# Performance work log

Measured on AMD Instinct MI355X. Metric: run time of the kernel, lower is better.

## Reference

```python
import jax, jax.numpy as jnp
import numpy as np

NUM_EXPERTS = 256
TOP_K = 8
N_GROUP = 8
TOPK_GROUP = 4
ROUTED_SCALING = 2.5
EXPERTS_PER_GROUP = NUM_EXPERTS // N_GROUP  # 32


def setup_inputs() -> dict:
    key = jax.random.key(0)
    k1, k2, k3 = jax.random.split(key, 3)
    hidden_states = jax.random.normal(k1, (8192, 7168), dtype=jnp.float32)
    weight = jax.random.normal(k2, (NUM_EXPERTS, 7168), dtype=jnp.float32) * 0.02
    e_score_correction_bias = jax.random.normal(k3, (NUM_EXPERTS,), dtype=jnp.float32) * 0.1
    return {
        "hidden_states": hidden_states,
        "weight": weight,
        "e_score_correction_bias": e_score_correction_bias,
    }


def reference(hidden_states, weight, e_score_correction_bias):
    # Router logits: [T, E]
    router_logits = jnp.einsum("th,eh->te", hidden_states, weight)
    scores = jax.nn.sigmoid(router_logits)
    scores_for_choice = scores + e_score_correction_bias  # [T, E]

    T = scores_for_choice.shape[0]
    # Group-limited selection (noaux_tc): group score = sum of top-2 experts in group
    grouped = scores_for_choice.reshape(T, N_GROUP, EXPERTS_PER_GROUP)
    group_top2, _ = jax.lax.top_k(grouped, 2)            # [T, G, 2]
    group_scores = group_top2.sum(axis=-1)               # [T, G]
    _, group_idx = jax.lax.top_k(group_scores, TOPK_GROUP)  # [T, topk_group]
    group_mask = jax.nn.one_hot(group_idx, N_GROUP, dtype=scores.dtype).max(axis=1)  # [T, G]
    expert_mask = jnp.repeat(group_mask, EXPERTS_PER_GROUP, axis=-1)  # [T, E]
    masked_scores = scores_for_choice * expert_mask

    # Final top-k experts; routing weights gathered from raw sigmoid scores
    _, selected_experts = jax.lax.top_k(masked_scores, TOP_K)         # [T, K] int32
    routing_weights = jnp.take_along_axis(scores, selected_experts, axis=-1)  # [T, K]
    routing_weights = routing_weights / (routing_weights.sum(axis=-1, keepdims=True) + 1e-20)
    routing_weights = routing_weights * ROUTED_SCALING
    return routing_weights, selected_experts
```

## Files before the change

### kernel.cpp

```cpp
#include <hip/hip_runtime.h>
#include <math.h>
#include <stdint.h>

#define T_TOK 8192
#define NEXP  256
#define HD    7168
#define PLANE ((size_t)T_TOK * NEXP)
#define SCALE 4096.0f
#define INV_S2 (1.0f / 16777216.0f)
#define BM 128
#define BK 32
#define NSTEP_TOT (HD / BK)
#define BIMG_STEP 32768

typedef _Float16 h8  __attribute__((ext_vector_type(8)));
typedef float f32x16 __attribute__((ext_vector_type(16)));
typedef __attribute__((address_space(3))) uint8_t       lds_t;
typedef __attribute__((address_space(1))) const uint8_t gbl_t;

__global__ __launch_bounds__(256) void wconv(const float* __restrict__ W,
                                             _Float16* __restrict__ img) {
  const int cc  = blockIdx.x * 256 + threadIdx.x;
  const int t   = cc >> 11;
  const int c   = cc & 2047;
  const int hl  = c >> 10;
  const int rem = c & 1023;
  const int row = rem >> 2;
  const int sp  = rem & 3;
  const int sl  = sp ^ ((row >> 1) & 3);
  const int k   = t * BK + sl * 8;

  const float* src = W + (size_t)row * HD + k;
  const float4 v0 = *(const float4*)src;
  const float4 v1 = *(const float4*)(src + 4);
  const float xs[8] = {v0.x, v0.y, v0.z, v0.w, v1.x, v1.y, v1.z, v1.w};
  h8 out;
#pragma unroll
  for (int j = 0; j < 8; ++j) {
    const float v = xs[j] * SCALE;
    const _Float16 hh = (_Float16)v;
    out[j] = hl ? (_Float16)(v - (float)hh) : hh;
  }
  *(h8*)(img + (size_t)cc * 8) = out;
}

__global__ __launch_bounds__(512) void router_gemm(
    const float* __restrict__ X, const _Float16* __restrict__ img,
    float* __restrict__ partial, int S) {
  __shared__ __align__(1024) _Float16 As[2][2][BM][BK];
  __shared__ __align__(1024) _Float16 Bs[2][2][NEXP][BK];

  const int tid = threadIdx.x;
  const int id  = blockIdx.x;
  const int sb  = id % S;
  const int mb  = id / S;

  const int row0  = mb * BM;
  const int nstep = (HD / S) / BK;
  const int tbase = sb * nstep;

  const int lane = tid & 63, wv = tid >> 6;
  const int wm = wv >> 2, wn = wv & 3;
  const int r31 = lane & 31, kg = lane >> 5;

  const int sm = tid >> 2;
  const int sk = tid & 3;
  const int spA = sk ^ ((sm >> 1) & 3);

  const float* Ap = X + (size_t)(row0 + sm) * HD + tbase * BK + sk * 8;
  const uint8_t* imgB = (const uint8_t*)img + (size_t)tbase * BIMG_STEP + tid * 16;

  f32x16 acc[2][2];
#pragma unroll
  for (int i = 0; i < 2; ++i)
#pragma unroll
    for (int j = 0; j < 2; ++j) acc[i][j] = (f32x16)(0.f);

#define STAGE_B(t, b)                                                          \
  {                                                                            \
    const uint8_t* g = imgB + (size_t)(t) * BIMG_STEP;                         \
    uint8_t* l = (uint8_t*)&Bs[b][0][0][0] + tid * 16;                         \
    _Pragma("unroll")                                                          \
    for (int i = 0; i < 4; ++i)                                                \
      __builtin_amdgcn_global_load_lds((gbl_t*)(uintptr_t)(g + i * 8192),      \
                                       (lds_t*)(uintptr_t)(l + i * 8192),      \
                                       16, 0, 0);                              \
  }

  STAGE_B(0, 0);
  {
    const float4 a0 = *(const float4*)(Ap);
    const float4 a1 = *(const float4*)(Ap + 4);
    const float xs[8] = {a0.x, a0.y, a0.z, a0.w, a1.x, a1.y, a1.z, a1.w};
    h8 hv, lv;
#pragma unroll
    for (int j = 0; j < 8; ++j) {
      const float v = xs[j] * SCALE;
      const _Float16 hh = (_Float16)v;
      hv[j] = hh; lv[j] = (_Float16)(v - (float)hh);
    }
    *(h8*)&As[0][0][sm][spA * 8] = hv;
    *(h8*)&As[0][1][sm][spA * 8] = lv;
  }

  for (int t = 0; t < nstep; ++t) {
    const int cur = t & 1;
    __syncthreads();

    const bool more = (t + 1 < nstep);
    float4 a0, a1;
    if (more) {
      STAGE_B(t + 1, cur ^ 1);
      a0 = *(const float4*)(Ap + (size_t)(t + 1) * BK);
      a1 = *(const float4*)(Ap + (size_t)(t + 1) * BK + 4);
    }

#pragma unroll
    for (int ks = 0; ks < 2; ++ks) {
      h8 aH[2], aL[2], bH[2], bL[2];
#pragma unroll
      for (int mi = 0; mi < 2; ++mi) {
        const int row = wm * 64 + mi * 32 + r31;
        const int sp  = (ks * 2 + kg) ^ ((row >> 1) & 3);
        aH[mi] = *(const h8*)&As[cur][0][row][sp * 8];
        aL[mi] = *(const h8*)&As[cur][1][row][sp * 8];
      }
#pragma unroll
      for (int ni = 0; ni < 2; ++ni) {
        const int col = wn * 64 + ni * 32 + r31;
        const int sp  = (ks * 2 + kg) ^ ((col >> 1) & 3);
        bH[ni] = *(const h8*)&Bs[cur][0][col][sp * 8];
        bL[ni] = *(const h8*)&Bs[cur][1][col][sp * 8];
      }
#pragma unroll
      for (int mi = 0; mi < 2; ++mi)
#pragma unroll
        for (int ni = 0; ni < 2; ++ni) {
          acc[mi][ni] = __builtin_amdgcn_mfma_f32_32x32x16_f16(aH[mi], bH[ni], acc[mi][ni], 0, 0, 0);
          acc[mi][ni] = __builtin_amdgcn_mfma_f32_32x32x16_f16(aL[mi], bH[ni], acc[mi][ni], 0, 0, 0);
          acc[mi][ni] = __builtin_amdgcn_mfma_f32_32x32x16_f16(aH[mi], bL[ni], acc[mi][ni], 0, 0, 0);
        }
    }

    if (more) {
      const int nb = cur ^ 1;
      const float xs[8] = {a0.x, a0.y, a0.z, a0.w, a1.x, a1.y, a1.z, a1.w};
      h8 hv, lv;
#pragma unroll
      for (int j = 0; j < 8; ++j) {
        const float v = xs[j] * SCALE;
        const _Float16 hh = (_Float16)v;
        hv[j] = hh; lv[j] = (_Float16)(v - (float)hh);
      }
      *(h8*)&As[nb][0][sm][spA * 8] = hv;
      *(h8*)&As[nb][1][sm][spA * 8] = lv;
    }
  }

  float* base = partial + (size_t)sb * PLANE;
#pragma unroll
  for (int mi = 0; mi < 2; ++mi)
#pragma unroll
    for (int ni = 0; ni < 2; ++ni) {
      const int col = wn * 64 + ni * 32 + r31;
#pragma unroll
      for (int reg = 0; reg < 16; ++reg) {
        const int rr  = (reg & 3) + 8 * (reg >> 2) + 4 * kg;
        const int row = row0 + wm * 64 + mi * 32 + rr;
        base[(size_t)row * NEXP + col] = acc[mi][ni][reg];
      }
    }
}

__global__ __launch_bounds__(256) void gate_kernel(const float* __restrict__ logits,
                                                   const float* __restrict__ bias,
                                                   float* __restrict__ out_w,
                                                   float* __restrict__ out_e, int S) {
    const int wave = threadIdx.x >> 6;
    const int lane = threadIdx.x & 63;
    const int t = blockIdx.x * 4 + wave;
    if (t >= T_TOK) return;

    float l4[4] = {0.f, 0.f, 0.f, 0.f};
    for (int s = 0; s < S; ++s) {
        const float4 v = *(const float4*)(&logits[(size_t)s * PLANE + (size_t)t * NEXP + lane * 4]);
        l4[0] += v.x; l4[1] += v.y; l4[2] += v.z; l4[3] += v.w;
    }
    const float4 bv = *(const float4*)(&bias[lane * 4]);

    float s4[4], c[4];
#pragma unroll
    for (int j = 0; j < 4; ++j) s4[j] = 1.f / (1.f + expf(-l4[j] * INV_S2));
    c[0] = s4[0] + bv.x;
    c[1] = s4[1] + bv.y;
    c[2] = s4[2] + bv.z;
    c[3] = s4[3] + bv.w;

    float a = fmaxf(c[0], c[1]), b = fminf(c[0], c[1]);
    float d = fmaxf(c[2], c[3]), e = fminf(c[2], c[3]);
    float m1 = fmaxf(a, d);
    float m2 = fmaxf(fminf(a, d), fmaxf(b, e));
#pragma unroll
    for (int off = 1; off < 8; off <<= 1) {
        const float o1 = __shfl_xor(m1, off);
        const float o2 = __shfl_xor(m2, off);
        const float n1 = fmaxf(m1, o1);
        const float n2 = fmaxf(fminf(m1, o1), fmaxf(m2, o2));
        m1 = n1; m2 = n2;
    }
    const float gs = m1 + m2;
    const int   g  = lane >> 3;

    int rank = 0;
#pragma unroll
    for (int gg = 0; gg < 8; ++gg) {
        const float og = __shfl(gs, gg * 8);
        rank += (og > gs) || (og == gs && gg < g);
    }
    const bool gsel = rank < 4;

    float v[4];
#pragma unroll
    for (int j = 0; j < 4; ++j) v[j] = gsel ? c[j] : 0.0f;

    float selw = 0.f;
    int   seli = 0;
    float wsum = 0.f;

#pragma unroll
    for (int k = 0; k < 8; ++k) {
        float bvv = v[0]; int bi = lane * 4; float br = s4[0];
#pragma unroll
        for (int j = 1; j < 4; ++j) {
            if (v[j] > bvv) { bvv = v[j]; bi = lane * 4 + j; br = s4[j]; }
        }
#pragma unroll
        for (int off = 32; off > 0; off >>= 1) {
            const float ov = __shfl_xor(bvv, off);
            const int   oi = __shfl_xor(bi, off);
            const float orr = __shfl_xor(br, off);
            if (ov > bvv || (ov == bvv && oi < bi)) { bvv = ov; bi = oi; br = orr; }
        }
        if (lane == k) { selw = br; seli = bi; }
        wsum += br;
        const int rem = bi - lane * 4;
#pragma unroll
        for (int j = 0; j < 4; ++j)
            if (rem == j) v[j] = -INFINITY;
    }

    if (lane < 8) {
        const float w = selw / (wsum + 1e-20f) * 2.5f;
        out_w[(size_t)t * 8 + lane] = w;
        out_e[(size_t)t * 8 + lane] = (float)seli;
    }
}

extern "C" void kernel_launch(void* const* d_in, const int* in_sizes, int n_in,
                              void* d_out, int out_size, void* d_ws, size_t ws_size,
                              hipStream_t stream) {
    const float* X    = (const float*)d_in[0];
    const float* W    = (const float*)d_in[1];
    const float* bias = (const float*)d_in[2];
    float* out = (float*)d_out;

    _Float16* img = (_Float16*)d_ws;
    const size_t woff = (size_t)NSTEP_TOT * BIMG_STEP;
    float* partial = (float*)((char*)d_ws + woff);

    int S = 1;
    if (ws_size >= woff + 4 * PLANE * sizeof(float)) S = 4;
    else if (ws_size >= woff + 2 * PLANE * sizeof(float)) S = 2;

    wconv<<<dim3(NSTEP_TOT * 2048 / 256), 256, 0, stream>>>(W, img);
    router_gemm<<<dim3((T_TOK / BM) * S), 512, 0, stream>>>(X, img, partial, S);
    gate_kernel<<<dim3(T_TOK / 4), 256, 0, stream>>>(partial, bias, out, out + (size_t)T_TOK * 8, S);
}
```

Before: 129.5 us.

## Split router GEMM tile along N into two 128-wide blocks with split accumulators

```diff
diff --git a/kernel.cpp b/kernel.cpp
--- a/kernel.cpp
+++ b/kernel.cpp
@@ -9,6 +9,7 @@
 #define SCALE 4096.0f
 #define INV_S2 (1.0f / 16777216.0f)
 #define BM 128
+#define BN 128
 #define BK 32
 #define NSTEP_TOT (HD / BK)
 #define BIMG_STEP 32768
@@ -23,14 +24,14 @@
   const int cc  = blockIdx.x * 256 + threadIdx.x;
   const int t   = cc >> 11;
   const int c   = cc & 2047;
-  const int hl  = c >> 10;
-  const int rem = c & 1023;
-  const int row = rem >> 2;
-  const int sp  = rem & 3;
+  const int nb  = c >> 10;
+  const int hl  = (c >> 9) & 1;
+  const int row = (c >> 2) & 127;
+  const int sp  = c & 3;
   const int sl  = sp ^ ((row >> 1) & 3);
   const int k   = t * BK + sl * 8;
 
-  const float* src = W + (size_t)row * HD + k;
+  const float* src = W + (size_t)(nb * 128 + row) * HD + k;
   const float4 v0 = *(const float4*)src;
   const float4 v1 = *(const float4*)(src + 4);
   const float xs[8] = {v0.x, v0.y, v0.z, v0.w, v1.x, v1.y, v1.z, v1.w};
@@ -44,37 +45,37 @@
   *(h8*)(img + (size_t)cc * 8) = out;
 }
 
-__global__ __launch_bounds__(512) void router_gemm(
+__global__ __launch_bounds__(256, 2) void router_gemm(
     const float* __restrict__ X, const _Float16* __restrict__ img,
     float* __restrict__ partial, int S) {
   __shared__ __align__(1024) _Float16 As[2][2][BM][BK];
-  __shared__ __align__(1024) _Float16 Bs[2][2][NEXP][BK];
+  __shared__ __align__(1024) _Float16 Bs[2][2][BN][BK];
 
   const int tid = threadIdx.x;
   const int id  = blockIdx.x;
   const int sb  = id % S;
-  const int mb  = id / S;
+  const int nb  = (id / S) & 1;
+  const int mb  = id / (2 * S);
 
   const int row0  = mb * BM;
   const int nstep = (HD / S) / BK;
   const int tbase = sb * nstep;
 
   const int lane = tid & 63, wv = tid >> 6;
-  const int wm = wv >> 2, wn = wv & 3;
+  const int wm = wv >> 1, wn = wv & 1;
   const int r31 = lane & 31, kg = lane >> 5;
 
-  const int sm = tid >> 2;
-  const int sk = tid & 3;
-  const int spA = sk ^ ((sm >> 1) & 3);
-
-  const float* Ap = X + (size_t)(row0 + sm) * HD + tbase * BK + sk * 8;
-  const uint8_t* imgB = (const uint8_t*)img + (size_t)tbase * BIMG_STEP + tid * 16;
-
-  f32x16 acc[2][2];
+  const int sm = tid >> 1;
+  const int sk = tid & 1;
+
+  const float* Ap = X + (size_t)(row0 + sm) * HD + tbase * BK + sk * 16;
+  const uint8_t* imgB = (const uint8_t*)img + (size_t)tbase * BIMG_STEP + nb * 16384 + tid * 16;
+
+  f32x16 accP[2][2], accQ[2][2];
 #pragma unroll
   for (int i = 0; i < 2; ++i)
 #pragma unroll
-    for (int j = 0; j < 2; ++j) acc[i][j] = (f32x16)(0.f);
+    for (int j = 0; j < 2; ++j) { accP[i][j] = (f32x16)(0.f); accQ[i][j] = (f32x16)(0.f); }
 
 #define STAGE_B(t, b)                                                          \
   {                                                                            \
@@ -82,25 +83,34 @@
     uint8_t* l = (uint8_t*)&Bs[b][0][0][0] + tid * 16;                         \
     _Pragma("unroll")                                                          \
     for (int i = 0; i < 4; ++i)                                                \
-      __builtin_amdgcn_global_load_lds((gbl_t*)(uintptr_t)(g + i * 8192),      \
-                                       (lds_t*)(uintptr_t)(l + i * 8192),      \
+      __builtin_amdgcn_global_load_lds((gbl_t*)(uintptr_t)(g + i * 4096),      \
+                                       (lds_t*)(uintptr_t)(l + i * 4096),      \
                                        16, 0, 0);                              \
+  }
+
+#define CVT_WRITE(b, s, va, vb)                                                \
+  {                                                                            \
+    const float xs[8] = {va.x, va.y, va.z, va.w, vb.x, vb.y, vb.z, vb.w};      \
+    h8 hv, lv_;                                                                \
+    _Pragma("unroll")                                                          \
+    for (int j = 0; j < 8; ++j) {                                              \
+      const float v = xs[j] * SCALE;                                           \
+      const _Float16 hh = (_Float16)v;                                         \
+      hv[j] = hh; lv_[j] = (_Float16)(v - (float)hh);                          \
+    }                                                                          \
+    const int spp = (s) ^ ((sm >> 1) & 3);                                     \
+    *(h8*)&As[b][0][sm][spp * 8] = hv;                                         \
+    *(h8*)&As[b][1][sm][spp * 8] = lv_;                                        \
   }
 
   STAGE_B(0, 0);
   {
     const float4 a0 = *(const float4*)(Ap);
     const float4 a1 = *(const float4*)(Ap + 4);
-    const float xs[8] = {a0.x, a0.y, a0.z, a0.w, a1.x, a1.y, a1.z, a1.w};
-    h8 hv, lv;
-#pragma unroll
-    for (int j = 0; j < 8; ++j) {
-      const float v = xs[j] * SCALE;
-      const _Float16 hh = (_Float16)v;
-      hv[j] = hh; lv[j] = (_Float16)(v - (float)hh);
-    }
-    *(h8*)&As[0][0][sm][spA * 8] = hv;
-    *(h8*)&As[0][1][sm][spA * 8] = lv;
+    const float4 a2 = *(const float4*)(Ap + 8);
+    const float4 a3 = *(const float4*)(Ap + 12);
+    CVT_WRITE(0, sk * 2,     a0, a1);
+    CVT_WRITE(0, sk * 2 + 1, a2, a3);
   }
 
   for (int t = 0; t < nstep; ++t) {
@@ -108,11 +118,14 @@
     __syncthreads();
 
     const bool more = (t + 1 < nstep);
-    float4 a0, a1;
+    float4 a0, a1, a2, a3;
     if (more) {
+      const float* ap = Ap + (size_t)(t + 1) * BK;
+      a0 = *(const float4*)(ap);
+      a1 = *(const float4*)(ap + 4);
+      a2 = *(const float4*)(ap + 8);
+      a3 = *(const float4*)(ap + 12);
       STAGE_B(t + 1, cur ^ 1);
-      a0 = *(const float4*)(Ap + (size_t)(t + 1) * BK);
-      a1 = *(const float4*)(Ap + (size_t)(t + 1) * BK + 4);
     }
 
 #pragma unroll
@@ -132,28 +145,29 @@
         bH[ni] = *(const h8*)&Bs[cur][0][col][sp * 8];
         bL[ni] = *(const h8*)&Bs[cur][1][col][sp * 8];
       }
+      __builtin_amdgcn_s_setprio(1);
 #pragma unroll
       for (int mi = 0; mi < 2; ++mi)
 #pragma unroll
-        for (int ni = 0; ni < 2; ++ni) {
-          acc[mi][ni] = __builtin_amdgcn_mfma_f32_32x32x16_f16(aH[mi], bH[ni], acc[mi][ni], 0, 0, 0);
-          acc[mi][ni] = __builtin_amdgcn_mfma_f32_32x32x16_f16(aL[mi], bH[ni], acc[mi][ni], 0, 0, 0);
-          acc[mi][ni] = __builtin_amdgcn_mfma_f32_32x32x16_f16(aH[mi], bL[ni], acc[mi][ni], 0, 0, 0);
-        }
+        for (int ni = 0; ni < 2; ++ni)
+          accP[mi][ni] = __builtin_amdgcn_mfma_f32_32x32x16_f16(aH[mi], bH[ni], accP[mi][ni], 0, 0, 0);
+#pragma unroll
+      for (int mi = 0; mi < 2; ++mi)
+#pragma unroll
+        for (int ni = 0; ni < 2; ++ni)
+          accQ[mi][ni] = __builtin_amdgcn_mfma_f32_32x32x16_f16(aL[mi], bH[ni], accQ[mi][ni], 0, 0, 0);
+#pragma unroll
+      for (int mi = 0; mi < 2; ++mi)
+#pragma unroll
+        for (int ni = 0; ni < 2; ++ni)
+          accQ[mi][ni] = __builtin_amdgcn_mfma_f32_32x32x16_f16(aH[mi], bL[ni], accQ[mi][ni], 0, 0, 0);
+      __builtin_amdgcn_s_setprio(0);
     }
 
     if (more) {
-      const int nb = cur ^ 1;
-      const float xs[8] = {a0.x, a0.y, a0.z, a0.w, a1.x, a1.y, a1.z, a1.w};
-      h8 hv, lv;
-#pragma unroll
-      for (int j = 0; j < 8; ++j) {
-        const float v = xs[j] * SCALE;
-        const _Float16 hh = (_Float16)v;
-        hv[j] = hh; lv[j] = (_Float16)(v - (float)hh);
-      }
-      *(h8*)&As[nb][0][sm][spA * 8] = hv;
-      *(h8*)&As[nb][1][sm][spA * 8] = lv;
+      const int nbuf = cur ^ 1;
+      CVT_WRITE(nbuf, sk * 2,     a0, a1);
+      CVT_WRITE(nbuf, sk * 2 + 1, a2, a3);
     }
   }
 
@@ -162,12 +176,13 @@
   for (int mi = 0; mi < 2; ++mi)
 #pragma unroll
     for (int ni = 0; ni < 2; ++ni) {
-      const int col = wn * 64 + ni * 32 + r31;
+      const f32x16 acc = accP[mi][ni] + accQ[mi][ni];
+      const int col = nb * BN + wn * 64 + ni * 32 + r31;
 #pragma unroll
       for (int reg = 0; reg < 16; ++reg) {
         const int rr  = (reg & 3) + 8 * (reg >> 2) + 4 * kg;
         const int row = row0 + wm * 64 + mi * 32 + rr;
-        base[(size_t)row * NEXP + col] = acc[mi][ni][reg];
+        base[(size_t)row * NEXP + col] = acc[reg];
       }
     }
 }
@@ -273,6 +288,6 @@
     else if (ws_size >= woff + 2 * PLANE * sizeof(float)) S = 2;
 
     wconv<<<dim3(NSTEP_TOT * 2048 / 256), 256, 0, stream>>>(W, img);
-    router_gemm<<<dim3((T_TOK / BM) * S), 512, 0, stream>>>(X, img, partial, S);
+    router_gemm<<<dim3((T_TOK / BM) * 2 * S), 256, 0, stream>>>(X, img, partial, S);
     gate_kernel<<<dim3(T_TOK / 4), 256, 0, stream>>>(partial, bias, out, out + (size_t)T_TOK * 8, S);
 }
```

Measured after the change: 145.7 us. +12.5%, slower.

## Restructure router GEMM main loop with split accumulators and explicit wait scheduling

Applied to the files above, without the earlier changes.

```diff
diff --git a/kernel.cpp b/kernel.cpp
--- a/kernel.cpp
+++ b/kernel.cpp
@@ -44,7 +44,7 @@
   *(h8*)(img + (size_t)cc * 8) = out;
 }
 
-__global__ __launch_bounds__(512) void router_gemm(
+__global__ __launch_bounds__(512, 2) void router_gemm(
     const float* __restrict__ X, const _Float16* __restrict__ img,
     float* __restrict__ partial, int S) {
   __shared__ __align__(1024) _Float16 As[2][2][BM][BK];
@@ -70,11 +70,11 @@
   const float* Ap = X + (size_t)(row0 + sm) * HD + tbase * BK + sk * 8;
   const uint8_t* imgB = (const uint8_t*)img + (size_t)tbase * BIMG_STEP + tid * 16;
 
-  f32x16 acc[2][2];
+  f32x16 accP[2][2], accQ[2][2];
 #pragma unroll
   for (int i = 0; i < 2; ++i)
 #pragma unroll
-    for (int j = 0; j < 2; ++j) acc[i][j] = (f32x16)(0.f);
+    for (int j = 0; j < 2; ++j) { accP[i][j] = (f32x16)(0.f); accQ[i][j] = (f32x16)(0.f); }
 
 #define STAGE_B(t, b)                                                          \
   {                                                                            \
@@ -87,74 +87,100 @@
                                        16, 0, 0);                              \
   }
 
-  STAGE_B(0, 0);
+#define CVT_WRITE_A(b, va, vb)                                                 \
+  {                                                                            \
+    const float xs[8] = {va.x, va.y, va.z, va.w, vb.x, vb.y, vb.z, vb.w};      \
+    h8 hv, lv_;                                                                \
+    _Pragma("unroll")                                                          \
+    for (int j = 0; j < 8; ++j) {                                              \
+      const float v = xs[j] * SCALE;                                           \
+      const _Float16 hh = (_Float16)v;                                         \
+      hv[j] = hh; lv_[j] = (_Float16)(v - (float)hh);                          \
+    }                                                                          \
+    *(h8*)&As[b][0][sm][spA * 8] = hv;                                         \
+    *(h8*)&As[b][1][sm][spA * 8] = lv_;                                        \
+  }
+
   {
     const float4 a0 = *(const float4*)(Ap);
     const float4 a1 = *(const float4*)(Ap + 4);
-    const float xs[8] = {a0.x, a0.y, a0.z, a0.w, a1.x, a1.y, a1.z, a1.w};
-    h8 hv, lv;
-#pragma unroll
-    for (int j = 0; j < 8; ++j) {
-      const float v = xs[j] * SCALE;
-      const _Float16 hh = (_Float16)v;
-      hv[j] = hh; lv[j] = (_Float16)(v - (float)hh);
-    }
-    *(h8*)&As[0][0][sm][spA * 8] = hv;
-    *(h8*)&As[0][1][sm][spA * 8] = lv;
+    __builtin_amdgcn_sched_barrier(0);
+    STAGE_B(0, 0);
+    asm volatile("s_waitcnt vmcnt(0)" ::: "memory");
+    __builtin_amdgcn_sched_barrier(0);
+    CVT_WRITE_A(0, a0, a1);
+    asm volatile("s_waitcnt lgkmcnt(0)" ::: "memory");
+    __builtin_amdgcn_s_barrier();
   }
 
   for (int t = 0; t < nstep; ++t) {
     const int cur = t & 1;
-    __syncthreads();
-
+    const int nxt = cur ^ 1;
     const bool more = (t + 1 < nstep);
+
     float4 a0, a1;
     if (more) {
-      STAGE_B(t + 1, cur ^ 1);
-      a0 = *(const float4*)(Ap + (size_t)(t + 1) * BK);
-      a1 = *(const float4*)(Ap + (size_t)(t + 1) * BK + 4);
-    }
-
+      const float* ap = Ap + (size_t)(t + 1) * BK;
+      a0 = *(const float4*)(ap);
+      a1 = *(const float4*)(ap + 4);
+      __builtin_amdgcn_sched_barrier(0);
+      STAGE_B(t + 1, nxt);
+      __builtin_amdgcn_sched_barrier(0);
+      asm volatile("s_waitcnt vmcnt(6)" ::: "memory");
+    } else {
+      asm volatile("s_waitcnt vmcnt(0)" ::: "memory");
+    }
+    __builtin_amdgcn_sched_barrier(0);
+
+    h8 aH[2][2], aL[2][2], bH[2][2], bL[2][2];
 #pragma unroll
     for (int ks = 0; ks < 2; ++ks) {
-      h8 aH[2], aL[2], bH[2], bL[2];
 #pragma unroll
       for (int mi = 0; mi < 2; ++mi) {
         const int row = wm * 64 + mi * 32 + r31;
         const int sp  = (ks * 2 + kg) ^ ((row >> 1) & 3);
-        aH[mi] = *(const h8*)&As[cur][0][row][sp * 8];
-        aL[mi] = *(const h8*)&As[cur][1][row][sp * 8];
+        aH[ks][mi] = *(const h8*)&As[cur][0][row][sp * 8];
+        aL[ks][mi] = *(const h8*)&As[cur][1][row][sp * 8];
       }
 #pragma unroll
       for (int ni = 0; ni < 2; ++ni) {
         const int col = wn * 64 + ni * 32 + r31;
         const int sp  = (ks * 2 + kg) ^ ((col >> 1) & 3);
-        bH[ni] = *(const h8*)&Bs[cur][0][col][sp * 8];
-        bL[ni] = *(const h8*)&Bs[cur][1][col][sp * 8];
+        bH[ks][ni] = *(const h8*)&Bs[cur][0][col][sp * 8];
+        bL[ks][ni] = *(const h8*)&Bs[cur][1][col][sp * 8];
       }
+    }
+    asm volatile("s_waitcnt lgkmcnt(0)" ::: "memory");
+    __builtin_amdgcn_sched_barrier(0);
+
+    __builtin_amdgcn_s_setprio(1);
+#pragma unroll
+    for (int ks = 0; ks < 2; ++ks) {
 #pragma unroll
       for (int mi = 0; mi < 2; ++mi)
 #pragma unroll
-        for (int ni = 0; ni < 2; ++ni) {
-          acc[mi][ni] = __builtin_amdgcn_mfma_f32_32x32x16_f16(aH[mi], bH[ni], acc[mi][ni], 0, 0, 0);
-          acc[mi][ni] = __builtin_amdgcn_mfma_f32_32x32x16_f16(aL[mi], bH[ni], acc[mi][ni], 0, 0, 0);
-          acc[mi][ni] = __builtin_amdgcn_mfma_f32_32x32x16_f16(aH[mi], bL[ni], acc[mi][ni], 0, 0, 0);
-        }
-    }
+        for (int ni = 0; ni < 2; ++ni)
+          accP[mi][ni] = __builtin_amdgcn_mfma_f32_32x32x16_f16(aH[ks][mi], bH[ks][ni], accP[mi][ni], 0, 0, 0);
+#pragma unroll
+      for (int mi = 0; mi < 2; ++mi)
+#pragma unroll
+        for (int ni = 0; ni < 2; ++ni)
+          accQ[mi][ni] = __builtin_amdgcn_mfma_f32_32x32x16_f16(aL[ks][mi], bH[ks][ni], accQ[mi][ni], 0, 0, 0);
+#pragma unroll
+      for (int mi = 0; mi < 2; ++mi)
+#pragma unroll
+        for (int ni = 0; ni < 2; ++ni)
+          accQ[mi][ni] = __builtin_amdgcn_mfma_f32_32x32x16_f16(aH[ks][mi], bL[ks][ni], accQ[mi][ni], 0, 0, 0);
+    }
+    __builtin_amdgcn_s_setprio(0);
 
     if (more) {
-      const int nb = cur ^ 1;
-      const float xs[8] = {a0.x, a0.y, a0.z, a0.w, a1.x, a1.y, a1.z, a1.w};
-      h8 hv, lv;
-#pragma unroll
-      for (int j = 0; j < 8; ++j) {
-        const float v = xs[j] * SCALE;
-        const _Float16 hh = (_Float16)v;
-        hv[j] = hh; lv[j] = (_Float16)(v - (float)hh);
-      }
-      *(h8*)&As[nb][0][sm][spA * 8] = hv;
-      *(h8*)&As[nb][1][sm][spA * 8] = lv;
-    }
+      asm volatile("s_waitcnt vmcnt(4)" ::: "memory");
+      __builtin_amdgcn_sched_barrier(0);
+      CVT_WRITE_A(nxt, a0, a1);
+    }
+    asm volatile("s_waitcnt lgkmcnt(0)" ::: "memory");
+    __builtin_amdgcn_s_barrier();
   }
 
   float* base = partial + (size_t)sb * PLANE;
@@ -162,12 +188,13 @@
   for (int mi = 0; mi < 2; ++mi)
 #pragma unroll
     for (int ni = 0; ni < 2; ++ni) {
+      const f32x16 acc = accP[mi][ni] + accQ[mi][ni];
       const int col = wn * 64 + ni * 32 + r31;
 #pragma unroll
       for (int reg = 0; reg < 16; ++reg) {
         const int rr  = (reg & 3) + 8 * (reg >> 2) + 4 * kg;
         const int row = row0 + wm * 64 + mi * 32 + rr;
-        base[(size_t)row * NEXP + col] = acc[mi][ni][reg];
+        base[(size_t)row * NEXP + col] = acc[reg];
       }
     }
 }
```

After: 131.2 us. No clear change (+1.3%).

## Double M tile to 256 and interleave LDS reads, loads and MFMA phases

Applied to the files above, without the earlier changes.

```diff
diff --git a/kernel.cpp b/kernel.cpp
--- a/kernel.cpp
+++ b/kernel.cpp
@@ -8,7 +8,7 @@
 #define PLANE ((size_t)T_TOK * NEXP)
 #define SCALE 4096.0f
 #define INV_S2 (1.0f / 16777216.0f)
-#define BM 128
+#define BM 256
 #define BK 32
 #define NSTEP_TOT (HD / BK)
 #define BIMG_STEP 32768
@@ -44,7 +44,7 @@
   *(h8*)(img + (size_t)cc * 8) = out;
 }
 
-__global__ __launch_bounds__(512) void router_gemm(
+__global__ __launch_bounds__(512, 2) void router_gemm(
     const float* __restrict__ X, const _Float16* __restrict__ img,
     float* __restrict__ partial, int S) {
   __shared__ __align__(1024) _Float16 As[2][2][BM][BK];
@@ -63,110 +63,171 @@
   const int wm = wv >> 2, wn = wv & 3;
   const int r31 = lane & 31, kg = lane >> 5;
 
-  const int sm = tid >> 2;
-  const int sk = tid & 3;
-  const int spA = sk ^ ((sm >> 1) & 3);
-
-  const float* Ap = X + (size_t)(row0 + sm) * HD + tbase * BK + sk * 8;
+  const int sm = tid >> 1;
+  const int sk = tid & 1;
+
+  const float* Ap = X + (size_t)(row0 + sm) * HD + tbase * BK + sk * 16;
   const uint8_t* imgB = (const uint8_t*)img + (size_t)tbase * BIMG_STEP + tid * 16;
 
-  f32x16 acc[2][2];
-#pragma unroll
-  for (int i = 0; i < 2; ++i)
+  f32x16 acc[4][2];
+#pragma unroll
+  for (int i = 0; i < 4; ++i)
 #pragma unroll
     for (int j = 0; j < 2; ++j) acc[i][j] = (f32x16)(0.f);
 
-#define STAGE_B(t, b)                                                          \
+#define LOAD_A(t)                                                              \
+  {                                                                            \
+    const float* ap = Ap + (size_t)(t) * BK;                                   \
+    a0 = *(const float4*)(ap);                                                 \
+    a1 = *(const float4*)(ap + 4);                                             \
+    a2 = *(const float4*)(ap + 8);                                             \
+    a3 = *(const float4*)(ap + 12);                                            \
+  }
+
+#define STAGE_B2(t, b, i0)                                                     \
   {                                                                            \
     const uint8_t* g = imgB + (size_t)(t) * BIMG_STEP;                         \
     uint8_t* l = (uint8_t*)&Bs[b][0][0][0] + tid * 16;                         \
-    _Pragma("unroll")                                                          \
-    for (int i = 0; i < 4; ++i)                                                \
-      __builtin_amdgcn_global_load_lds((gbl_t*)(uintptr_t)(g + i * 8192),      \
-                                       (lds_t*)(uintptr_t)(l + i * 8192),      \
-                                       16, 0, 0);                              \
-  }
-
-  STAGE_B(0, 0);
+    __builtin_amdgcn_global_load_lds((gbl_t*)(uintptr_t)(g + (i0) * 8192),     \
+                                     (lds_t*)(uintptr_t)(l + (i0) * 8192), 16, 0, 0); \
+    __builtin_amdgcn_global_load_lds((gbl_t*)(uintptr_t)(g + ((i0) + 1) * 8192), \
+                                     (lds_t*)(uintptr_t)(l + ((i0) + 1) * 8192), 16, 0, 0); \
+  }
+
+#define CVT_WRITE_A(b)                                                         \
+  {                                                                            \
+    const float xs[16] = {a0.x, a0.y, a0.z, a0.w, a1.x, a1.y, a1.z, a1.w,      \
+                          a2.x, a2.y, a2.z, a2.w, a3.x, a3.y, a3.z, a3.w};     \
+    h8 hv0, hv1, lv0, lv1;                                                     \
+    _Pragma("unroll")                                                          \
+    for (int j = 0; j < 8; ++j) {                                              \
+      const float v = xs[j] * SCALE;                                           \
+      const _Float16 hh = (_Float16)v;                                         \
+      hv0[j] = hh; lv0[j] = (_Float16)(v - (float)hh);                         \
+    }                                                                          \
+    _Pragma("unroll")                                                          \
+    for (int j = 0; j < 8; ++j) {                                              \
+      const float v = xs[8 + j] * SCALE;                                       \
+      const _Float16 hh = (_Float16)v;                                         \
+      hv1[j] = hh; lv1[j] = (_Float16)(v - (float)hh);                         \
+    }                                                                          \
+    const int s0 = (sk * 2) ^ ((sm >> 1) & 3);                                 \
+    const int s1 = (sk * 2 + 1) ^ ((sm >> 1) & 3);                             \
+    *(h8*)&As[b][0][sm][s0 * 8] = hv0;                                         \
+    *(h8*)&As[b][0][sm][s1 * 8] = hv1;                                         \
+    *(h8*)&As[b][1][sm][s0 * 8] = lv0;                                         \
+    *(h8*)&As[b][1][sm][s1 * 8] = lv1;                                         \
+  }
+
+#define READ_B(ks, dst)                                                        \
+  _Pragma("unroll")                                                            \
+  for (int ni = 0; ni < 2; ++ni)                                               \
+    _Pragma("unroll")                                                          \
+    for (int pl = 0; pl < 2; ++pl) {                                           \
+      const int col = wn * 64 + ni * 32 + r31;                                 \
+      const int sp  = ((ks) * 2 + kg) ^ ((col >> 1) & 3);                      \
+      dst[ni][pl] = *(const h8*)&Bs[cur][pl][col][sp * 8];                     \
+    }
+
+#define READ_A(ks, mbase, dst)                                                 \
+  _Pragma("unroll")                                                            \
+  for (int mi = 0; mi < 2; ++mi)                                               \
+    _Pragma("unroll")                                                          \
+    for (int pl = 0; pl < 2; ++pl) {                                           \
+      const int row = wm * 128 + ((mbase) + mi) * 32 + r31;                    \
+      const int sp  = ((ks) * 2 + kg) ^ ((row >> 1) & 3);                      \
+      dst[mi][pl] = *(const h8*)&As[cur][pl][row][sp * 8];                     \
+    }
+
+#define MFMA12(aF, bF, mbase)                                                  \
+  __builtin_amdgcn_s_setprio(1);                                               \
+  _Pragma("unroll")                                                            \
+  for (int mi = 0; mi < 2; ++mi)                                               \
+    _Pragma("unroll")                                                          \
+    for (int ni = 0; ni < 2; ++ni)                                             \
+      acc[(mbase) + mi][ni] = __builtin_amdgcn_mfma_f32_32x32x16_f16(          \
+          aF[mi][0], bF[ni][0], acc[(mbase) + mi][ni], 0, 0, 0);               \
+  _Pragma("unroll")                                                            \
+  for (int mi = 0; mi < 2; ++mi)                                               \
+    _Pragma("unroll")                                                          \
+    for (int ni = 0; ni < 2; ++ni)                                             \
+      acc[(mbase) + mi][ni] = __builtin_amdgcn_mfma_f32_32x32x16_f16(          \
+          aF[mi][1], bF[ni][0], acc[(mbase) + mi][ni], 0, 0, 0);               \
+  _Pragma("unroll")                                                            \
+  for (int mi = 0; mi < 2; ++mi)                                               \
+    _Pragma("unroll")                                                          \
+    for (int ni = 0; ni < 2; ++ni)                                             \
+      acc[(mbase) + mi][ni] = __builtin_amdgcn_mfma_f32_32x32x16_f16(          \
+          aF[mi][0], bF[ni][1], acc[(mbase) + mi][ni], 0, 0, 0);               \
+  __builtin_amdgcn_s_setprio(0);
+
+#define FENCE asm volatile("" ::: "memory");
+#define BAR   __builtin_amdgcn_s_barrier();
+#define WAITL0 asm volatile("s_waitcnt lgkmcnt(0)" ::: "memory"); __builtin_amdgcn_sched_barrier(0);
+
   {
-    const float4 a0 = *(const float4*)(Ap);
-    const float4 a1 = *(const float4*)(Ap + 4);
-    const float xs[8] = {a0.x, a0.y, a0.z, a0.w, a1.x, a1.y, a1.z, a1.w};
-    h8 hv, lv;
-#pragma unroll
-    for (int j = 0; j < 8; ++j) {
-      const float v = xs[j] * SCALE;
-      const _Float16 hh = (_Float16)v;
-      hv[j] = hh; lv[j] = (_Float16)(v - (float)hh);
-    }
-    *(h8*)&As[0][0][sm][spA * 8] = hv;
-    *(h8*)&As[0][1][sm][spA * 8] = lv;
+    float4 a0, a1, a2, a3;
+    LOAD_A(0);
+    STAGE_B2(0, 0, 0);
+    STAGE_B2(0, 0, 2);
+    asm volatile("s_waitcnt vmcnt(4)" ::: "memory");
+    CVT_WRITE_A(0);
+    asm volatile("s_waitcnt vmcnt(0) lgkmcnt(0)" ::: "memory");
+    BAR;
   }
 
   for (int t = 0; t < nstep; ++t) {
     const int cur = t & 1;
-    __syncthreads();
-
+    const int nxt = cur ^ 1;
     const bool more = (t + 1 < nstep);
-    float4 a0, a1;
+
+    h8 b0[2][2], b1[2][2], aA[2][2], aB[2][2];
+    float4 a0, a1, a2, a3;
+
+    READ_B(0, b0);
+    READ_A(0, 0, aA);
+    if (more) LOAD_A(t + 1);
+    FENCE; BAR; WAITL0;
+    MFMA12(aA, b0, 0);
+    FENCE; BAR;
+
+    READ_A(0, 2, aB);
+    if (more) STAGE_B2(t + 1, nxt, 0);
+    FENCE; BAR; WAITL0;
+    MFMA12(aB, b0, 2);
+    FENCE; BAR;
+
+    READ_B(1, b1);
+    READ_A(1, 0, aA);
+    if (more) STAGE_B2(t + 1, nxt, 2);
+    FENCE; BAR; WAITL0;
+    MFMA12(aA, b1, 0);
+    FENCE; BAR;
+
+    READ_A(1, 2, aB);
     if (more) {
-      STAGE_B(t + 1, cur ^ 1);
-      a0 = *(const float4*)(Ap + (size_t)(t + 1) * BK);
-      a1 = *(const float4*)(Ap + (size_t)(t + 1) * BK + 4);
-    }
-
-#pragma unroll
-    for (int ks = 0; ks < 2; ++ks) {
-      h8 aH[2], aL[2], bH[2], bL[2];
-#pragma unroll
-      for (int mi = 0; mi < 2; ++mi) {
-        const int row = wm * 64 + mi * 32 + r31;
-        const int sp  = (ks * 2 + kg) ^ ((row >> 1) & 3);
-        aH[mi] = *(const h8*)&As[cur][0][row][sp * 8];
-        aL[mi] = *(const h8*)&As[cur][1][row][sp * 8];
-      }
-#pragma unroll
-      for (int ni = 0; ni < 2; ++ni) {
-        const int col = wn * 64 + ni * 32 + r31;
-        const int sp  = (ks * 2 + kg) ^ ((col >> 1) & 3);
-        bH[ni] = *(const h8*)&Bs[cur][0][col][sp * 8];
-        bL[ni] = *(const h8*)&Bs[cur][1][col][sp * 8];
-      }
-#pragma unroll
-      for (int mi = 0; mi < 2; ++mi)
-#pragma unroll
-        for (int ni = 0; ni < 2; ++ni) {
-          acc[mi][ni] = __builtin_amdgcn_mfma_f32_32x32x16_f16(aH[mi], bH[ni], acc[mi][ni], 0, 0, 0);
-          acc[mi][ni] = __builtin_amdgcn_mfma_f32_32x32x16_f16(aL[mi], bH[ni], acc[mi][ni], 0, 0, 0);
-          acc[mi][ni] = __builtin_amdgcn_mfma_f32_32x32x16_f16(aH[mi], bL[ni], acc[mi][ni], 0, 0, 0);
-        }
-    }
-
-    if (more) {
-      const int nb = cur ^ 1;
-      const float xs[8] = {a0.x, a0.y, a0.z, a0.w, a1.x, a1.y, a1.z, a1.w};
-      h8 hv, lv;
-#pragma unroll
-      for (int j = 0; j < 8; ++j) {
-        const float v = xs[j] * SCALE;
-        const _Float16 hh = (_Float16)v;
-        hv[j] = hh; lv[j] = (_Float16)(v - (float)hh);
-      }
-      *(h8*)&As[nb][0][sm][spA * 8] = hv;
-      *(h8*)&As[nb][1][sm][spA * 8] = lv;
-    }
+      asm volatile("s_waitcnt vmcnt(4)" ::: "memory");
+      __builtin_amdgcn_sched_barrier(0);
+      CVT_WRITE_A(nxt);
+    }
+    asm volatile("s_waitcnt lgkmcnt(0)" ::: "memory");
+    __builtin_amdgcn_sched_barrier(0);
+    BAR;
+    MFMA12(aB, b1, 2);
+    if (more) asm volatile("s_waitcnt vmcnt(0)" ::: "memory");
+    FENCE; BAR;
   }
 
   float* base = partial + (size_t)sb * PLANE;
 #pragma unroll
-  for (int mi = 0; mi < 2; ++mi)
+  for (int mi = 0; mi < 4; ++mi)
 #pragma unroll
     for (int ni = 0; ni < 2; ++ni) {
       const int col = wn * 64 + ni * 32 + r31;
 #pragma unroll
       for (int reg = 0; reg < 16; ++reg) {
         const int rr  = (reg & 3) + 8 * (reg >> 2) + 4 * kg;
-        const int row = row0 + wm * 64 + mi * 32 + rr;
+        const int row = row0 + wm * 128 + mi * 32 + rr;
         base[(size_t)row * NEXP + col] = acc[mi][ni][reg];
       }
     }
@@ -269,7 +330,8 @@
     float* partial = (float*)((char*)d_ws + woff);
 
     int S = 1;
-    if (ws_size >= woff + 4 * PLANE * sizeof(float)) S = 4;
+    if (ws_size >= woff + 8 * PLANE * sizeof(float)) S = 8;
+    else if (ws_size >= woff + 4 * PLANE * sizeof(float)) S = 4;
     else if (ws_size >= woff + 2 * PLANE * sizeof(float)) S = 2;
 
     wconv<<<dim3(NSTEP_TOT * 2048 / 256), 256, 0, stream>>>(W, img);
```

New measurement: 135.2 us. 4.4% more time.
